# Performance work log

Measured on AMD Instinct MI355X. Metric: run time of the kernel, lower is better.

The kernel has to match this reference:

```python
import jax, jax.numpy as jnp
import numpy as np

D_MODEL, H, D_FF = 1024, 16, 4096
D_K = D_MODEL // H
EPS = 1e-5


def _layernorm(x, alpha, bias):
    # faithful to source: unbiased std (ddof=1), eps added to std (not var)
    mean = jnp.mean(x, axis=-1, keepdims=True)
    std = jnp.std(x, axis=-1, keepdims=True, ddof=1)
    return alpha * (x - mean) / (std + EPS) + bias


def setup_inputs() -> dict:
    key = jax.random.key(0)
    ks = jax.random.split(key, 12)
    B, S = 2, 2048
    s = 1.0 / np.sqrt(D_MODEL)
    inp = {
        "x": jax.random.normal(ks[0], (B, S, D_MODEL), dtype=jnp.float32),
        "mask": jnp.ones((B, 1, 1, S), dtype=jnp.int32),
        "wq": jax.random.normal(ks[1], (D_MODEL, D_MODEL), dtype=jnp.float32) * s,
        "wk": jax.random.normal(ks[2], (D_MODEL, D_MODEL), dtype=jnp.float32) * s,
        "wv": jax.random.normal(ks[3], (D_MODEL, D_MODEL), dtype=jnp.float32) * s,
        "wo": jax.random.normal(ks[4], (D_MODEL, D_MODEL), dtype=jnp.float32) * s,
        "w1": jax.random.normal(ks[5], (D_MODEL, D_FF), dtype=jnp.float32) * s,
        "b1": jnp.zeros((D_FF,), dtype=jnp.float32),
        "w2": jax.random.normal(ks[6], (D_FF, D_MODEL), dtype=jnp.float32) * (1.0 / np.sqrt(D_FF)),
        "b2": jnp.zeros((D_MODEL,), dtype=jnp.float32),
        "alpha1": jnp.ones((1,), dtype=jnp.float32),
        "bias1": jnp.zeros((1,), dtype=jnp.float32),
        "alpha2": jnp.ones((1,), dtype=jnp.float32),
        "bias2": jnp.zeros((1,), dtype=jnp.float32),
    }
    return inp


def reference(x, mask, wq, wk, wv, wo, w1, b1, w2, b2, alpha1, bias1, alpha2, bias2):
    B, S, _ = x.shape

    # --- sublayer 1: pre-norm self-attention + residual ---
    xn = _layernorm(x, alpha1, bias1)
    q = (xn @ wq).reshape(B, S, H, D_K).transpose(0, 2, 1, 3)  # [B,H,S,Dk]
    k = (xn @ wk).reshape(B, S, H, D_K).transpose(0, 2, 1, 3)
    v = (xn @ wv).reshape(B, S, H, D_K).transpose(0, 2, 1, 3)

    scores = jnp.einsum("bhqd,bhkd->bhqk", q, k) / np.sqrt(D_K)  # [B,H,S,S]
    scores = jnp.where(mask == 0, jnp.float32(-1e9), scores)
    attn = jax.nn.softmax(scores, axis=-1)
    ctx = jnp.einsum("bhqk,bhkd->bhqd", attn, v)
    ctx = ctx.transpose(0, 2, 1, 3).reshape(B, S, D_MODEL)
    x = x + ctx @ wo

    # --- sublayer 2: pre-norm FFN + residual ---
    xn = _layernorm(x, alpha2, bias2)
    h = jax.nn.relu(xn @ w1 + b1)
    x = x + h @ w2 + b2
    return x
```

## Files before the change

### kernel.cpp

```cpp
#include <hip/hip_runtime.h>
#include <hip/hip_bf16.h>

typedef __attribute__((ext_vector_type(8))) short bf16x8;
typedef __attribute__((ext_vector_type(4))) short short4v;
typedef __attribute__((ext_vector_type(4))) float floatx4;

#define MFMA16(A, B, C) __builtin_amdgcn_mfma_f32_16x16x32_bf16((A), (B), (C), 0, 0, 0)

__device__ inline short bf16bits(float f) {
  __hip_bfloat16 h = __float2bfloat16(f);
  return *reinterpret_cast<short*>(&h);
}
__device__ inline unsigned cvtpk(float lo, float hi) {
  unsigned r;
  asm("v_cvt_pk_bf16_f32 %0, %1, %2" : "=v"(r) : "v"(lo), "v"(hi));
  return r;
}
typedef __attribute__((address_space(3))) char lds_char;
typedef __attribute__((address_space(1))) const char glob_char;
__device__ inline void gll16(const void* g, void* l) {
  __builtin_amdgcn_global_load_lds((glob_char*)g, (lds_char*)l, 16, 0, 0);
}

__global__ __launch_bounds__(256) void transpose_f2b_kernel(
    const float* __restrict__ src, __hip_bfloat16* __restrict__ dst,
    int R, int C, int ldS) {
  __shared__ __align__(16) __hip_bfloat16 tile[64][72];
  const long r0 = (long)blockIdx.y * 64, c0 = (long)blockIdx.x * 64;
  for (int i = threadIdx.x; i < 1024; i += 256) {
    int r = i >> 4, c4 = (i & 15) * 4;
    float4 f = *(const float4*)&src[(r0 + r) * ldS + c0 + c4];
    short4v s;
    s[0] = bf16bits(f.x); s[1] = bf16bits(f.y);
    s[2] = bf16bits(f.z); s[3] = bf16bits(f.w);
    *(short4v*)&tile[r][c4] = s;
  }
  __syncthreads();
  for (int i = threadIdx.x; i < 512; i += 256) {
    int c = i >> 3, r8 = (i & 7) * 8;
    bf16x8 sv;
#pragma unroll
    for (int j = 0; j < 8; j++) sv[j] = *reinterpret_cast<const short*>(&tile[r8 + j][c]);
    *(bf16x8*)&dst[(c0 + c) * R + r0 + r8] = sv;
  }
}

__global__ __launch_bounds__(256) void transpose_qkv_kernel(
    const float* __restrict__ wq, const float* __restrict__ wk,
    const float* __restrict__ wv, __hip_bfloat16* __restrict__ wqkvT) {
  __shared__ __align__(16) __hip_bfloat16 tile[64][72];
  const int which = blockIdx.y >> 4;
  const float* src = which == 0 ? wq : (which == 1 ? wk : wv);
  __hip_bfloat16* dst = wqkvT + (size_t)which * 1024 * 1024;
  const long r0 = (long)(blockIdx.y & 15) * 64, c0 = (long)blockIdx.x * 64;
  for (int i = threadIdx.x; i < 1024; i += 256) {
    int r = i >> 4, c4 = (i & 15) * 4;
    float4 f = *(const float4*)&src[(r0 + r) * 1024 + c0 + c4];
    short4v s;
    s[0] = bf16bits(f.x); s[1] = bf16bits(f.y);
    s[2] = bf16bits(f.z); s[3] = bf16bits(f.w);
    *(short4v*)&tile[r][c4] = s;
  }
  __syncthreads();
  for (int i = threadIdx.x; i < 512; i += 256) {
    int c = i >> 3, r8 = (i & 7) * 8;
    bf16x8 sv;
#pragma unroll
    for (int j = 0; j < 8; j++) sv[j] = *reinterpret_cast<const short*>(&tile[r8 + j][c]);
    *(bf16x8*)&dst[(c0 + c) * 1024 + r0 + r8] = sv;
  }
}

__global__ __launch_bounds__(256) void vtrans_kernel(
    const __hip_bfloat16* __restrict__ qkv, __hip_bfloat16* __restrict__ vt) {
  __shared__ __align__(16) __hip_bfloat16 tile[64][72];
  const int bh = blockIdx.y, b = bh >> 4, h = bh & 15;
  const long s0 = (long)blockIdx.x * 64;
  const __hip_bfloat16* src = qkv + ((long)b * 2048 + s0) * 3072 + 2048 + h * 64;
  for (int i = threadIdx.x; i < 512; i += 256) {
    int s = i >> 3, d8 = (i & 7) * 8;
    *(uint4*)&tile[s][d8] = *(const uint4*)&src[(long)s * 3072 + d8];
  }
  __syncthreads();
  __hip_bfloat16* dstb = vt + (long)bh * 64 * 2048 + s0;
  for (int i = threadIdx.x; i < 512; i += 256) {
    int d = i >> 3, s8 = (i & 7) * 8;
    bf16x8 sv;
#pragma unroll
    for (int j = 0; j < 8; j++) sv[j] = *reinterpret_cast<const short*>(&tile[s8 + j][d]);
    *(bf16x8*)&dstb[(long)d * 2048 + s8] = sv;
  }
}

__global__ __launch_bounds__(256) void mask2add_kernel(
    const int* __restrict__ mask, float* __restrict__ addm,
    int* __restrict__ flags) {
  const int i = blockIdx.x * 256 + threadIdx.x;
  const int mv = mask[i];
  addm[i] = mv ? 0.f : -1e30f;
  __shared__ int ok[4];
  const unsigned long long bal = __ballot(mv != 0);
  if ((threadIdx.x & 63) == 0) ok[threadIdx.x >> 6] = (bal == ~0ull) ? 1 : 0;
  __syncthreads();
  if (threadIdx.x == 0) flags[blockIdx.x] = ok[0] & ok[1] & ok[2] & ok[3];
}

__global__ __launch_bounds__(256) void bias_add_kernel(
    const float* __restrict__ x1, const float* __restrict__ b2,
    float* __restrict__ out) {
  const int i = (blockIdx.x * 256 + threadIdx.x) * 4;
  float4 v = *(const float4*)&x1[i];
  const float4 bb = *(const float4*)&b2[i & 1023];
  v.x += bb.x; v.y += bb.y; v.z += bb.z; v.w += bb.w;
  *(float4*)&out[i] = v;
}

__global__ __launch_bounds__(256) void ln_kernel(
    const float* __restrict__ x, __hip_bfloat16* __restrict__ y,
    const float* __restrict__ alpha_p, const float* __restrict__ bias_p) {
  __shared__ float sred[8];
  const long row = blockIdx.x;
  const int t = threadIdx.x;
  const float* xr = x + row * 1024;
  float v[4];
#pragma unroll
  for (int i = 0; i < 4; i++) v[i] = xr[t * 4 + i];
  float sum = 0.f, sq = 0.f;
#pragma unroll
  for (int i = 0; i < 4; i++) { sum += v[i]; sq += v[i] * v[i]; }
#pragma unroll
  for (int off = 32; off; off >>= 1) {
    sum += __shfl_down(sum, off);
    sq += __shfl_down(sq, off);
  }
  if ((t & 63) == 0) { sred[(t >> 6) * 2] = sum; sred[(t >> 6) * 2 + 1] = sq; }
  __syncthreads();
  sum = sred[0] + sred[2] + sred[4] + sred[6];
  sq = sred[1] + sred[3] + sred[5] + sred[7];
  const float mean = sum * (1.f / 1024.f);
  float var = (sq - 1024.f * mean * mean) * (1.f / 1023.f);
  var = fmaxf(var, 0.f);
  const float denom = sqrtf(var) + 1e-5f;
  const float sc = alpha_p[0] / denom;
  const float beta = bias_p[0];
  __hip_bfloat16* yr = y + row * 1024;
#pragma unroll
  for (int i = 0; i < 4; i++) yr[t * 4 + i] = __float2bfloat16((v[i] - mean) * sc + beta);
}

template <int EPI>
__global__ __launch_bounds__(256) void gemm_bt_kernel(
    const __hip_bfloat16* __restrict__ A, const __hip_bfloat16* __restrict__ Bt,
    void* __restrict__ Cv, const float* __restrict__ bias,
    const float* __restrict__ res, int M, int N, int K) {
  __shared__ __align__(16) __hip_bfloat16 lA[128 * 32];
  __shared__ __align__(16) __hip_bfloat16 lB[128 * 32];
  const int tid = threadIdx.x;
  const int wave = tid >> 6, lane = tid & 63;
  const int quad = lane >> 4, l16 = lane & 15;
  const int wm = wave >> 1, wn = wave & 1;
  const long m0 = (long)blockIdx.y * 128;
  const long n0 = (long)blockIdx.x * 128;

  const int rA0 = tid >> 2, cA0 = (tid & 3) * 8;
  const int rA1 = (tid + 256) >> 2, cA1 = ((tid + 256) & 3) * 8;

  floatx4 acc[4][4];
#pragma unroll
  for (int i = 0; i < 4; i++)
#pragma unroll
    for (int j = 0; j < 4; j++) acc[i][j] = (floatx4){0.f, 0.f, 0.f, 0.f};

  const __hip_bfloat16* Ab = A + m0 * K;
  const __hip_bfloat16* Bb = Bt + n0 * K;

  for (int k0 = 0; k0 < K; k0 += 32) {
    __syncthreads();
    gll16(&Ab[(long)rA0 * K + k0 + cA0], &lA[wave * 512]);
    gll16(&Ab[(long)rA1 * K + k0 + cA1], &lA[2048 + wave * 512]);
    gll16(&Bb[(long)rA0 * K + k0 + cA0], &lB[wave * 512]);
    gll16(&Bb[(long)rA1 * K + k0 + cA1], &lB[2048 + wave * 512]);
    __syncthreads();
    bf16x8 af[4], bfr[4];
#pragma unroll
    for (int mi = 0; mi < 4; mi++)
      af[mi] = *(const bf16x8*)&lA[(wm * 64 + mi * 16 + l16) * 32 + quad * 8];
#pragma unroll
    for (int ni = 0; ni < 4; ni++)
      bfr[ni] = *(const bf16x8*)&lB[(wn * 64 + ni * 16 + l16) * 32 + quad * 8];
#pragma unroll
    for (int mi = 0; mi < 4; mi++)
#pragma unroll
      for (int ni = 0; ni < 4; ni++)
        acc[mi][ni] = MFMA16(af[mi], bfr[ni], acc[mi][ni]);
  }

#pragma unroll
  for (int mi = 0; mi < 4; mi++) {
#pragma unroll
    for (int ni = 0; ni < 4; ni++) {
#pragma unroll
      for (int r = 0; r < 4; r++) {
        const long row = m0 + wm * 64 + mi * 16 + quad * 4 + r;
        const long col = n0 + wn * 64 + ni * 16 + l16;
        const long idx = row * N + col;
        float v = acc[mi][ni][r];
        if (EPI == 0) {
          ((__hip_bfloat16*)Cv)[idx] = __float2bfloat16(v);
        } else if (EPI == 1) {
          ((float*)Cv)[idx] = v + res[idx];
        } else if (EPI == 2) {
          v += bias[col];
          ((__hip_bfloat16*)Cv)[idx] = __float2bfloat16(fmaxf(v, 0.f));
        } else if (EPI == 3) {
          float* Cf = (float*)Cv;
          Cf[idx] = Cf[idx] + v;
        }
      }
    }
  }
}

template <int EPI>
__global__ __launch_bounds__(256) void gemm64_bt_kernel(
    const __hip_bfloat16* __restrict__ A, const __hip_bfloat16* __restrict__ Bt,
    void* __restrict__ Cv, const float* __restrict__ bias,
    const float* __restrict__ res, int M, int N, int K) {
  __shared__ __align__(16) __hip_bfloat16 lA[128 * 32];
  __shared__ __align__(16) __hip_bfloat16 lB[64 * 32];
  const int tid = threadIdx.x;
  const int wave = tid >> 6, lane = tid & 63;
  const int quad = lane >> 4, l16 = lane & 15;
  const int wm = wave >> 1, wn = wave & 1;
  const long m0 = (long)blockIdx.y * 128;
  const long n0 = (long)blockIdx.x * 64;

  const int rA0 = tid >> 2, cA0 = (tid & 3) * 8;
  const int rA1 = (tid + 256) >> 2, cA1 = ((tid + 256) & 3) * 8;

  floatx4 acc[4][2];
#pragma unroll
  for (int i = 0; i < 4; i++)
#pragma unroll
    for (int j = 0; j < 2; j++) acc[i][j] = (floatx4){0.f, 0.f, 0.f, 0.f};

  const __hip_bfloat16* Ab = A + m0 * K;
  const __hip_bfloat16* Bb = Bt + n0 * K;

  for (int k0 = 0; k0 < K; k0 += 32) {
    __syncthreads();
    gll16(&Ab[(long)rA0 * K + k0 + cA0], &lA[wave * 512]);
    gll16(&Ab[(long)rA1 * K + k0 + cA1], &lA[2048 + wave * 512]);
    gll16(&Bb[(long)rA0 * K + k0 + cA0], &lB[wave * 512]);
    __syncthreads();
    bf16x8 af[4], bfr[2];
#pragma unroll
    for (int mi = 0; mi < 4; mi++)
      af[mi] = *(const bf16x8*)&lA[(wm * 64 + mi * 16 + l16) * 32 + quad * 8];
#pragma unroll
    for (int ni = 0; ni < 2; ni++)
      bfr[ni] = *(const bf16x8*)&lB[(wn * 32 + ni * 16 + l16) * 32 + quad * 8];
#pragma unroll
    for (int mi = 0; mi < 4; mi++)
#pragma unroll
      for (int ni = 0; ni < 2; ni++)
        acc[mi][ni] = MFMA16(af[mi], bfr[ni], acc[mi][ni]);
  }

#pragma unroll
  for (int mi = 0; mi < 4; mi++) {
#pragma unroll
    for (int ni = 0; ni < 2; ni++) {
#pragma unroll
      for (int r = 0; r < 4; r++) {
        const long row = m0 + wm * 64 + mi * 16 + quad * 4 + r;
        const long col = n0 + wn * 32 + ni * 16 + l16;
        const long idx = row * N + col;
        float v = acc[mi][ni][r];
        if (EPI == 1) {
          ((float*)Cv)[idx] = v + res[idx];
        } else if (EPI == 3) {
          float* Cf = (float*)Cv;
          Cf[idx] = Cf[idx] + v;
        }
      }
    }
  }
}

__global__ __launch_bounds__(256) void attn_kernel(
    const __hip_bfloat16* __restrict__ qkv, const __hip_bfloat16* __restrict__ vt,
    const float* __restrict__ addm, const int* __restrict__ flags,
    __hip_bfloat16* __restrict__ ctx) {
  __shared__ __align__(16) __hip_bfloat16 lK[64 * 64];
  __shared__ __align__(16) __hip_bfloat16 lV[64 * 64];
  const int tid = threadIdx.x, wave = tid >> 6, lane = tid & 63;
  const int quad = lane >> 4, l16 = lane & 15;
  const int bh = blockIdx.y, b = bh >> 4, h = bh & 15;
  const int q0 = blockIdx.x * 64 + wave * 16;
  const float cs = 0.18033688011112042f;
  const float inv_cs = 5.545177444479562f;

  const __hip_bfloat16* kb = qkv + (long)b * 2048 * 3072 + 1024 + h * 64;
  const __hip_bfloat16* vb = vt + (long)bh * 64 * 2048;
  const float* am = addm + b * 2048;

  int fm = 1;
#pragma unroll
  for (int i = 0; i < 8; ++i) fm &= flags[b * 8 + i];
  const bool fast = (fm != 0);

  const long qoff = ((long)b * 2048 + q0 + l16) * 3072 + h * 64;
  const bf16x8 bq0 = *(const bf16x8*)&qkv[qoff + quad * 8];
  const bf16x8 bq1 = *(const bf16x8*)&qkv[qoff + 32 + quad * 8];

  const int srow = lane >> 3;
  const int cslot = lane & 7;
  const int cg = cslot ^ srow;

  floatx4 o[4];
#pragma unroll
  for (int mi = 0; mi < 4; mi++) o[mi] = (floatx4){0.f, 0.f, 0.f, 0.f};
  float mrow = -3.0e38f, lrow = 0.f;

  for (int t = 0; t < 32; ++t) {
    __syncthreads();
#pragma unroll
    for (int j = 0; j < 2; ++j) {
      const int rloc = wave * 16 + j * 8 + srow;
      gll16(kb + (long)(t * 64 + rloc) * 3072 + cg * 8,
            &lK[(wave * 16 + j * 8) * 64]);
      gll16(vb + (long)rloc * 2048 + t * 64 + cg * 8,
            &lV[(wave * 16 + j * 8) * 64]);
    }
    __syncthreads();

    floatx4 c[4];
    __builtin_amdgcn_s_setprio(1);
#pragma unroll
    for (int g = 0; g < 4; ++g) {
      const bf16x8 a0 =
          *(const bf16x8*)&lK[(g * 16 + l16) * 64 + ((quad) ^ (l16 & 7)) * 8];
      const bf16x8 a1 =
          *(const bf16x8*)&lK[(g * 16 + l16) * 64 + ((4 + quad) ^ (l16 & 7)) * 8];
      floatx4 cc = {0.f, 0.f, 0.f, 0.f};
      cc = MFMA16(a0, bq0, cc);
      cc = MFMA16(a1, bq1, cc);
      c[g] = cc;
    }
    __builtin_amdgcn_s_setprio(0);

    if (!fast) {
#pragma unroll
      for (int g = 0; g < 4; ++g) {
        const float4 a4 = *(const float4*)&am[t * 64 + g * 16 + quad * 4];
        c[g][0] = fmaf(a4.x, inv_cs, c[g][0]);
        c[g][1] = fmaf(a4.y, inv_cs, c[g][1]);
        c[g][2] = fmaf(a4.z, inv_cs, c[g][2]);
        c[g][3] = fmaf(a4.w, inv_cs, c[g][3]);
      }
    }

    const float m0 = fmaxf(fmaxf(c[0][0], c[0][1]), c[0][2]);
    const float m1 = fmaxf(fmaxf(c[0][3], c[1][0]), c[1][1]);
    const float m2 = fmaxf(fmaxf(c[1][2], c[1][3]), c[2][0]);
    const float m3 = fmaxf(fmaxf(c[2][1], c[2][2]), c[2][3]);
    const float m4 = fmaxf(fmaxf(c[3][0], c[3][1]), c[3][2]);
    float tm = fmaxf(fmaxf(fmaxf(m0, m1), fmaxf(m2, m3)), fmaxf(m4, c[3][3]));
    tm = fmaxf(tm, __shfl_xor(tm, 16));
    tm = fmaxf(tm, __shfl_xor(tm, 32));
    const float tms = tm * cs;

    if (__any(tms > mrow + 8.f)) {
      const float mnew = fmaxf(mrow, tms);
      const float alpha = exp2f(mrow - mnew);
      mrow = mnew;
      lrow *= alpha;
#pragma unroll
      for (int mi = 0; mi < 4; mi++) o[mi] *= alpha;
    }

    const float mneg = -mrow;
    float p[4][4];
#pragma unroll
    for (int g = 0; g < 4; ++g)
#pragma unroll
      for (int r = 0; r < 4; ++r)
        p[g][r] = exp2f(fmaf(c[g][r], cs, mneg));
    const float s0 = (p[0][0] + p[0][1]) + (p[0][2] + p[0][3]);
    const float s1 = (p[1][0] + p[1][1]) + (p[1][2] + p[1][3]);
    const float s2 = (p[2][0] + p[2][1]) + (p[2][2] + p[2][3]);
    const float s3 = (p[3][0] + p[3][1]) + (p[3][2] + p[3][3]);
    float rs = (s0 + s1) + (s2 + s3);
    rs += __shfl_xor(rs, 16);
    rs += __shfl_xor(rs, 32);
    lrow += rs;

    unsigned dw[4][2];
#pragma unroll
    for (int g = 0; g < 4; ++g) {
      dw[g][0] = cvtpk(p[g][0], p[g][1]);
      dw[g][1] = cvtpk(p[g][2], p[g][3]);
    }
    const int qs0 = (quad & 1) * 2;
    const int src0 = l16 + 16 * qs0, src1 = src0 + 16;
    const bool hig = (quad >> 1) != 0;
#pragma unroll
    for (int ss = 0; ss < 2; ++ss) {
      const unsigned a0 = __shfl((int)dw[2 * ss][0], src0);
      const unsigned b0 = __shfl((int)dw[2 * ss + 1][0], src0);
      const unsigned a1 = __shfl((int)dw[2 * ss][1], src0);
      const unsigned b1 = __shfl((int)dw[2 * ss + 1][1], src0);
      const unsigned a2 = __shfl((int)dw[2 * ss][0], src1);
      const unsigned b2 = __shfl((int)dw[2 * ss + 1][0], src1);
      const unsigned a3 = __shfl((int)dw[2 * ss][1], src1);
      const unsigned b3 = __shfl((int)dw[2 * ss + 1][1], src1);
      uint4 du;
      du.x = hig ? b0 : a0;
      du.y = hig ? b1 : a1;
      du.z = hig ? b2 : a2;
      du.w = hig ? b3 : a3;
      const bf16x8 bp = *reinterpret_cast<bf16x8*>(&du);
      __builtin_amdgcn_s_setprio(1);
#pragma unroll
      for (int mi = 0; mi < 4; ++mi) {
        const bf16x8 av = *(const bf16x8*)&lV[(mi * 16 + l16) * 64 +
                                              ((ss * 4 + quad) ^ (l16 & 7)) * 8];
        o[mi] = MFMA16(av, bp, o[mi]);
      }
      __builtin_amdgcn_s_setprio(0);
    }
  }

  const float inv_l = 1.f / lrow;
  const long cb = ((long)b * 2048 + q0 + l16) * 1024 + h * 64;
#pragma unroll
  for (int mi = 0; mi < 4; mi++) {
    uint2 st;
    st.x = cvtpk(o[mi][0] * inv_l, o[mi][1] * inv_l);
    st.y = cvtpk(o[mi][2] * inv_l, o[mi][3] * inv_l);
    *(uint2*)&ctx[cb + mi * 16 + quad * 4] = st;
  }
}

extern "C" void kernel_launch(void* const* d_in, const int* in_sizes, int n_in,
                              void* d_out, int out_size, void* d_ws, size_t ws_size,
                              hipStream_t stream) {
  const float* x = (const float*)d_in[0];
  const int* mask = (const int*)d_in[1];
  const float* wq = (const float*)d_in[2];
  const float* wk = (const float*)d_in[3];
  const float* wv = (const float*)d_in[4];
  const float* wo = (const float*)d_in[5];
  const float* w1 = (const float*)d_in[6];
  const float* b1 = (const float*)d_in[7];
  const float* w2 = (const float*)d_in[8];
  const float* b2 = (const float*)d_in[9];
  const float* alpha1 = (const float*)d_in[10];
  const float* bias1 = (const float*)d_in[11];
  const float* alpha2 = (const float*)d_in[12];
  const float* bias2 = (const float*)d_in[13];

  char* ws = (char*)d_ws;
  char* dob = (char*)d_out;
  const size_t MiB = 1048576;
  __hip_bfloat16* qkv   = (__hip_bfloat16*)(ws + 0);
  __hip_bfloat16* wqkvT = (__hip_bfloat16*)(ws + 24 * MiB);
  __hip_bfloat16* vtb   = (__hip_bfloat16*)(ws + 24 * MiB);
  float*          x1    = (float*)(ws + 0);
  __hip_bfloat16* hc    = (__hip_bfloat16*)(ws + 16 * MiB);
  __hip_bfloat16* xn    = (__hip_bfloat16*)d_out;
  __hip_bfloat16* ctxb  = (__hip_bfloat16*)d_out;
  __hip_bfloat16* xn2   = (__hip_bfloat16*)d_out;
  __hip_bfloat16* woT   = (__hip_bfloat16*)(dob + 8 * MiB);
  __hip_bfloat16* w1Th  = (__hip_bfloat16*)(dob + 8 * MiB);
  __hip_bfloat16* w2Th  = (__hip_bfloat16*)(dob + 12 * MiB);
  float*          addm  = (float*)(dob + 12 * MiB);
  int*            flags = (int*)(dob + 12 * MiB + 16 * 1024);

  const dim3 b256(256);
  const dim3 g1k(16, 16);
  transpose_qkv_kernel<<<dim3(16, 48), b256, 0, stream>>>(wq, wk, wv, wqkvT);
  ln_kernel<<<4096, b256, 0, stream>>>(x, xn, alpha1, bias1);
  gemm_bt_kernel<0><<<dim3(24, 32), b256, 0, stream>>>(xn, wqkvT, qkv, nullptr, nullptr,
                                                       4096, 3072, 1024);
  vtrans_kernel<<<dim3(32, 32), b256, 0, stream>>>(qkv, vtb);
  mask2add_kernel<<<16, b256, 0, stream>>>(mask, addm, flags);
  attn_kernel<<<dim3(32, 32), b256, 0, stream>>>(qkv, vtb, addm, flags, ctxb);
  transpose_f2b_kernel<<<g1k, b256, 0, stream>>>(wo, woT, 1024, 1024, 1024);
  gemm64_bt_kernel<1><<<dim3(16, 32), b256, 0, stream>>>(ctxb, woT, x1, nullptr, x,
                                                         4096, 1024, 1024);
  ln_kernel<<<4096, b256, 0, stream>>>(x1, xn2, alpha2, bias2);
  for (int c = 0; c < 2; ++c) {
    transpose_f2b_kernel<<<dim3(32, 16), b256, 0, stream>>>(w1 + c * 2048, w1Th,
                                                            1024, 2048, 4096);
    gemm_bt_kernel<2><<<dim3(16, 32), b256, 0, stream>>>(xn2, w1Th, hc, b1 + c * 2048,
                                                         nullptr, 4096, 2048, 1024);
    transpose_f2b_kernel<<<dim3(16, 32), b256, 0, stream>>>(w2 + (size_t)c * 2048 * 1024,
                                                            w2Th, 2048, 1024, 1024);
    gemm64_bt_kernel<3><<<dim3(16, 32), b256, 0, stream>>>(hc, w2Th, x1, nullptr,
                                                           nullptr, 4096, 1024, 2048);
  }
  bias_add_kernel<<<4096, b256, 0, stream>>>(x1, b2, (float*)d_out);
}
```

Baseline: 471.1 us.

## Double-buffer K/V tiles in attention and use native exp2 intrinsic

```diff
diff --git a/kernel.cpp b/kernel.cpp
--- a/kernel.cpp
+++ b/kernel.cpp
@@ -292,8 +292,8 @@
     const __hip_bfloat16* __restrict__ qkv, const __hip_bfloat16* __restrict__ vt,
     const float* __restrict__ addm, const int* __restrict__ flags,
     __hip_bfloat16* __restrict__ ctx) {
-  __shared__ __align__(16) __hip_bfloat16 lK[64 * 64];
-  __shared__ __align__(16) __hip_bfloat16 lV[64 * 64];
+  __shared__ __align__(16) __hip_bfloat16 lK[2][64 * 64];
+  __shared__ __align__(16) __hip_bfloat16 lV[2][64 * 64];
   const int tid = threadIdx.x, wave = tid >> 6, lane = tid & 63;
   const int quad = lane >> 4, l16 = lane & 15;
   const int bh = blockIdx.y, b = bh >> 4, h = bh & 15;
@@ -317,32 +317,45 @@
   const int srow = lane >> 3;
   const int cslot = lane & 7;
   const int cg = cslot ^ srow;
+  const int rbase = wave * 16 + srow;
 
   floatx4 o[4];
 #pragma unroll
   for (int mi = 0; mi < 4; mi++) o[mi] = (floatx4){0.f, 0.f, 0.f, 0.f};
   float mrow = -3.0e38f, lrow = 0.f;
 
+#pragma unroll
+  for (int j = 0; j < 2; ++j) {
+    const int rloc = rbase + j * 8;
+    gll16(kb + (long)rloc * 3072 + cg * 8, &lK[0][(wave * 16 + j * 8) * 64]);
+    gll16(vb + (long)rloc * 2048 + cg * 8, &lV[0][(wave * 16 + j * 8) * 64]);
+  }
+
+  int cur = 0;
   for (int t = 0; t < 32; ++t) {
     __syncthreads();
-#pragma unroll
-    for (int j = 0; j < 2; ++j) {
-      const int rloc = wave * 16 + j * 8 + srow;
-      gll16(kb + (long)(t * 64 + rloc) * 3072 + cg * 8,
-            &lK[(wave * 16 + j * 8) * 64]);
-      gll16(vb + (long)rloc * 2048 + t * 64 + cg * 8,
-            &lV[(wave * 16 + j * 8) * 64]);
-    }
-    __syncthreads();
+    if (t + 1 < 32) {
+      const int nxt = cur ^ 1;
+#pragma unroll
+      for (int j = 0; j < 2; ++j) {
+        const int rloc = rbase + j * 8;
+        gll16(kb + (long)((t + 1) * 64 + rloc) * 3072 + cg * 8,
+              &lK[nxt][(wave * 16 + j * 8) * 64]);
+        gll16(vb + (long)rloc * 2048 + (t + 1) * 64 + cg * 8,
+              &lV[nxt][(wave * 16 + j * 8) * 64]);
+      }
+    }
+    const __hip_bfloat16* lKc = lK[cur];
+    const __hip_bfloat16* lVc = lV[cur];
 
     floatx4 c[4];
     __builtin_amdgcn_s_setprio(1);
 #pragma unroll
     for (int g = 0; g < 4; ++g) {
       const bf16x8 a0 =
-          *(const bf16x8*)&lK[(g * 16 + l16) * 64 + ((quad) ^ (l16 & 7)) * 8];
+          *(const bf16x8*)&lKc[(g * 16 + l16) * 64 + ((quad) ^ (l16 & 7)) * 8];
       const bf16x8 a1 =
-          *(const bf16x8*)&lK[(g * 16 + l16) * 64 + ((4 + quad) ^ (l16 & 7)) * 8];
+          *(const bf16x8*)&lKc[(g * 16 + l16) * 64 + ((4 + quad) ^ (l16 & 7)) * 8];
       floatx4 cc = {0.f, 0.f, 0.f, 0.f};
       cc = MFMA16(a0, bq0, cc);
       cc = MFMA16(a1, bq1, cc);
@@ -373,7 +386,7 @@
 
     if (__any(tms > mrow + 8.f)) {
       const float mnew = fmaxf(mrow, tms);
-      const float alpha = exp2f(mrow - mnew);
+      const float alpha = __builtin_amdgcn_exp2f(mrow - mnew);
       mrow = mnew;
       lrow *= alpha;
 #pragma unroll
@@ -386,7 +399,7 @@
     for (int g = 0; g < 4; ++g)
 #pragma unroll
       for (int r = 0; r < 4; ++r)
-        p[g][r] = exp2f(fmaf(c[g][r], cs, mneg));
+        p[g][r] = __builtin_amdgcn_exp2f(fmaf(c[g][r], cs, mneg));
     const float s0 = (p[0][0] + p[0][1]) + (p[0][2] + p[0][3]);
     const float s1 = (p[1][0] + p[1][1]) + (p[1][2] + p[1][3]);
     const float s2 = (p[2][0] + p[2][1]) + (p[2][2] + p[2][3]);
@@ -424,12 +437,13 @@
       __builtin_amdgcn_s_setprio(1);
 #pragma unroll
       for (int mi = 0; mi < 4; ++mi) {
-        const bf16x8 av = *(const bf16x8*)&lV[(mi * 16 + l16) * 64 +
-                                              ((ss * 4 + quad) ^ (l16 & 7)) * 8];
+        const bf16x8 av = *(const bf16x8*)&lVc[(mi * 16 + l16) * 64 +
+                                               ((ss * 4 + quad) ^ (l16 & 7)) * 8];
         o[mi] = MFMA16(av, bp, o[mi]);
       }
       __builtin_amdgcn_s_setprio(0);
     }
+    cur ^= 1;
   }
 
   const float inv_l = 1.f / lrow;
```

New measurement: 457.9 us. -2.8%, faster.
